# Performance work log

Measured on AMD Instinct MI355X. Metric: run time of the kernel, lower is better.

## Reference

```python
import jax, jax.numpy as jnp
import numpy as np
import math

WINDOW_SIZE = 11
SIGMA = 1.5
K1 = 0.01
K2 = 0.03
MAX_VAL = 1.0


def _make_window(window_size=WINDOW_SIZE, sigma=SIGMA):
    # Faithful to torch: 1D gaussian -> [1,1,window_size] -> repeat((3,1,1,1)) -> [3,1,1,ws]
    xs = np.arange(window_size)
    w = np.exp(-((xs - window_size // 2) ** 2) / float(2 * sigma ** 2)).astype(np.float32)
    w = w / w.sum()
    w = w[None, None, :]                      # [1,1,ws]
    w = np.tile(w[None], (3, 1, 1, 1))        # [3,1,1,ws]  (OIHW, 1x11 kernel, 3 out channels)
    return jnp.asarray(w)


def _conv(x, w, pad):
    # x: [B,1,H,W], w: [3,1,1,ws], padding=pad on both spatial dims (matches torch conv2d)
    return jax.lax.conv_general_dilated(
        x, w, window_strides=(1, 1), padding=((pad, pad), (pad, pad)),
        dimension_numbers=("NCHW", "OIHW", "NCHW"))


def setup_inputs() -> dict:
    key = jax.random.key(0)
    k1, k2 = jax.random.split(key)
    B, H, W = 16, 512, 512
    img1 = jax.random.uniform(k1, (B, H, W), dtype=jnp.float32)
    img2 = jax.random.uniform(k2, (B, H, W), dtype=jnp.float32)
    return {"img1": img1, "img2": img2}


def reference(img1, img2):
    pad = WINDOW_SIZE // 2
    window = _make_window()
    x1 = img1[:, None, :, :]  # [B,1,H,W]
    x2 = img2[:, None, :, :]

    mu1 = _conv(x1, window, pad)              # [B,3,H+2p,W]
    mu2 = _conv(x2, window, pad)
    mu1_mu2 = mu1 * mu2
    mu1_sq = mu1 * mu1
    mu2_sq = mu2 * mu2
    sigma1_sq = _conv(x1 * x1, window, pad) - mu1_sq
    sigma2_sq = _conv(x2 * x2, window, pad) - mu2_sq
    sigma12 = _conv(x1 * x2, window, pad) - mu1_mu2

    C1 = (K1 * MAX_VAL) ** 2
    C2 = (K2 * MAX_VAL) ** 2
    ssim = (2 * mu1_mu2 + C1) * (2 * sigma12 + C2) / (
        (mu1_sq + mu2_sq + C1) * (sigma1_sq + sigma2_sq + C2))
    return 1.0 - jnp.mean(ssim)
```

## Files before the change

kernel.cpp:

```cpp
#include <hip/hip_runtime.h>
#include <cmath>

typedef float f32x2 __attribute__((ext_vector_type(2)));
typedef float f32x4 __attribute__((ext_vector_type(4)));

#define IMG_W 512
#define NROWS 8192
#define PAIRS_PER_BLOCK 2
#define NBLOCKS (NROWS / (2 * PAIRS_PER_BLOCK))
#define TPB 128

struct WinW { float w[11]; };

__global__ __launch_bounds__(TPB) void ssim_rows(
    const float* __restrict__ img1, const float* __restrict__ img2,
    float* __restrict__ partial, WinW ww)
{
    __shared__ __align__(16) f32x2 l1[528];
    __shared__ __align__(16) f32x2 l2[528];
    const int tid = threadIdx.x;

    const float C1 = 1e-4f;
    const float C2 = 9e-4f;

    f32x2 acc = {0.f, 0.f};

    for (int pp = 0; pp < PAIRS_PER_BLOCK; ++pp) {
        const int pairIdx = blockIdx.x * PAIRS_PER_BLOCK + pp;
        const long long r0 = (long long)pairIdx * 2 * IMG_W;
        const int col = 4 * tid;

        const f32x4 a0 = *(const f32x4*)&img1[r0 + col];
        const f32x4 a1 = *(const f32x4*)&img1[r0 + IMG_W + col];
        const f32x4 b0 = *(const f32x4*)&img2[r0 + col];
        const f32x4 b1 = *(const f32x4*)&img2[r0 + IMG_W + col];

        __syncthreads();
        #pragma unroll
        for (int c = 0; c < 4; ++c) {
            l1[5 + col + c] = f32x2{a0[c], a1[c]};
            l2[5 + col + c] = f32x2{b0[c], b1[c]};
        }
        if (tid < 16) {
            const int slot = (tid < 5) ? tid : (512 + tid);
            l1[slot] = f32x2{0.f, 0.f};
            l2[slot] = f32x2{0.f, 0.f};
        }
        __syncthreads();

        f32x2 a[16], b[16];
        #pragma unroll
        for (int s = 0; s < 8; ++s) {
            *(f32x4*)&a[2 * s] = *(const f32x4*)&l1[col + 2 * s];
            *(f32x4*)&b[2 * s] = *(const f32x4*)&l2[col + 2 * s];
        }

        f32x2 mu1[4], mu2[4], s11[4], s22[4], s12[4];
        #pragma unroll
        for (int p = 0; p < 4; ++p) {
            mu1[p] = f32x2{0.f, 0.f}; mu2[p] = f32x2{0.f, 0.f};
            s11[p] = f32x2{0.f, 0.f}; s22[p] = f32x2{0.f, 0.f};
            s12[p] = f32x2{0.f, 0.f};
        }

        #pragma unroll
        for (int j = 0; j < 14; ++j) {
            const f32x2 aj = a[j], bj = b[j];
            const f32x2 aa = aj * aj, bb = bj * bj, ab = aj * bj;
            #pragma unroll
            for (int p = 0; p < 4; ++p) {
                const int k = j - p;
                if (k >= 0 && k < 11) {
                    const float wk = ww.w[k];
                    mu1[p] += wk * aj;
                    mu2[p] += wk * bj;
                    s11[p] += wk * aa;
                    s22[p] += wk * bb;
                    s12[p] += wk * ab;
                }
            }
        }

        #pragma unroll
        for (int p = 0; p < 4; ++p) {
            const f32x2 m12 = mu1[p] * mu2[p];
            const f32x2 m1s = mu1[p] * mu1[p];
            const f32x2 m2s = mu2[p] * mu2[p];
            const f32x2 num = (2.f * m12 + C1) * (2.f * (s12[p] - m12) + C2);
            const f32x2 den = (m1s + m2s + C1) * ((s11[p] - m1s) + (s22[p] - m2s) + C2);
            f32x2 r;
            r.x = __builtin_amdgcn_rcpf(den.x);
            r.y = __builtin_amdgcn_rcpf(den.y);
            acc += num * r;
        }
    }

    float s = acc.x + acc.y;
    #pragma unroll
    for (int off = 32; off > 0; off >>= 1)
        s += __shfl_down(s, off, 64);
    __shared__ float wsum[TPB / 64];
    if ((tid & 63) == 0) wsum[tid >> 6] = s;
    __syncthreads();
    if (tid == 0) partial[blockIdx.x] = wsum[0] + wsum[1];
}

__global__ __launch_bounds__(256) void ssim_final(
    const float* __restrict__ partial, float* __restrict__ out)
{
    const int tid = threadIdx.x;
    float s = 0.f;
    for (int i = tid; i < NBLOCKS; i += 256) s += partial[i];
    #pragma unroll
    for (int off = 32; off > 0; off >>= 1)
        s += __shfl_down(s, off, 64);
    __shared__ float ws[4];
    if ((tid & 63) == 0) ws[tid >> 6] = s;
    __syncthreads();
    if (tid == 0) {
        const float total = ws[0] + ws[1] + ws[2] + ws[3];
        out[0] = 1.0f - (total + 81920.0f) / 4276224.0f;
    }
}

extern "C" void kernel_launch(void* const* d_in, const int* in_sizes, int n_in,
                              void* d_out, int out_size, void* d_ws, size_t ws_size,
                              hipStream_t stream) {
    const float* img1 = (const float*)d_in[0];
    const float* img2 = (const float*)d_in[1];
    float* out = (float*)d_out;
    float* partial = (float*)d_ws;

    WinW ww;
    for (int i = 0; i < 11; ++i) {
        const double d = (double)(i - 5);
        ww.w[i] = (float)std::exp(-(d * d) / 4.5);
    }
    float s = 0.f;
    for (int i = 0; i < 11; ++i) s += ww.w[i];
    for (int i = 0; i < 11; ++i) ww.w[i] /= s;

    ssim_rows<<<NBLOCKS, TPB, 0, stream>>>(img1, img2, partial, ww);
    ssim_final<<<1, 256, 0, stream>>>(partial, out);
}
```

Before: 16.38 us.

## Fuse final reduction via fixed-point atomics and prefetch next row pair

Drops the separate final-reduction kernel. Each block converts its partial sum to a 64-bit fixed-point integer and atomically adds it, and the last block to arrive (tracked by an atomic counter) writes the result. The per-block loop now prefetches the next row pair into registers and double-buffers shared memory, which removes one barrier per iteration, and each block handles twice as many row pairs. A memset is added to the stream to clear the accumulator. Risks include the extra memset launch cost and the limited precision of the fixed-point conversion.

Result: slower. 40.86 us (+149.4%).

```diff
diff --git a/kernel.cpp b/kernel.cpp
--- a/kernel.cpp
+++ b/kernel.cpp
@@ -6,53 +6,63 @@
 
 #define IMG_W 512
 #define NROWS 8192
-#define PAIRS_PER_BLOCK 2
+#define PAIRS_PER_BLOCK 4
 #define NBLOCKS (NROWS / (2 * PAIRS_PER_BLOCK))
 #define TPB 128
+#define SCALE 16777216.0
 
 struct WinW { float w[11]; };
 
-__global__ __launch_bounds__(TPB) void ssim_rows(
+__global__ __launch_bounds__(TPB) void ssim_fused(
     const float* __restrict__ img1, const float* __restrict__ img2,
-    float* __restrict__ partial, WinW ww)
+    unsigned long long* __restrict__ acc64, unsigned int* __restrict__ cnt,
+    float* __restrict__ out, WinW ww)
 {
-    __shared__ __align__(16) f32x2 l1[528];
-    __shared__ __align__(16) f32x2 l2[528];
+    __shared__ __align__(16) f32x2 l1[2][528];
+    __shared__ __align__(16) f32x2 l2[2][528];
     const int tid = threadIdx.x;
-
+    const int col = 4 * tid;
     const float C1 = 1e-4f;
     const float C2 = 9e-4f;
 
     f32x2 acc = {0.f, 0.f};
 
+    const long long base = (long long)blockIdx.x * (PAIRS_PER_BLOCK * 2) * IMG_W;
+
+    f32x4 pa0 = *(const f32x4*)&img1[base + col];
+    f32x4 pa1 = *(const f32x4*)&img1[base + IMG_W + col];
+    f32x4 pb0 = *(const f32x4*)&img2[base + col];
+    f32x4 pb1 = *(const f32x4*)&img2[base + IMG_W + col];
+
+    #pragma unroll
     for (int pp = 0; pp < PAIRS_PER_BLOCK; ++pp) {
-        const int pairIdx = blockIdx.x * PAIRS_PER_BLOCK + pp;
-        const long long r0 = (long long)pairIdx * 2 * IMG_W;
-        const int col = 4 * tid;
+        const int buf = pp & 1;
+        const f32x4 a0 = pa0, a1 = pa1, b0 = pb0, b1 = pb1;
+        if (pp + 1 < PAIRS_PER_BLOCK) {
+            const long long nb = base + (long long)(pp + 1) * 2 * IMG_W;
+            pa0 = *(const f32x4*)&img1[nb + col];
+            pa1 = *(const f32x4*)&img1[nb + IMG_W + col];
+            pb0 = *(const f32x4*)&img2[nb + col];
+            pb1 = *(const f32x4*)&img2[nb + IMG_W + col];
+        }
 
-        const f32x4 a0 = *(const f32x4*)&img1[r0 + col];
-        const f32x4 a1 = *(const f32x4*)&img1[r0 + IMG_W + col];
-        const f32x4 b0 = *(const f32x4*)&img2[r0 + col];
-        const f32x4 b1 = *(const f32x4*)&img2[r0 + IMG_W + col];
-
-        __syncthreads();
         #pragma unroll
         for (int c = 0; c < 4; ++c) {
-            l1[5 + col + c] = f32x2{a0[c], a1[c]};
-            l2[5 + col + c] = f32x2{b0[c], b1[c]};
+            l1[buf][5 + col + c] = f32x2{a0[c], a1[c]};
+            l2[buf][5 + col + c] = f32x2{b0[c], b1[c]};
         }
         if (tid < 16) {
             const int slot = (tid < 5) ? tid : (512 + tid);
-            l1[slot] = f32x2{0.f, 0.f};
-            l2[slot] = f32x2{0.f, 0.f};
+            l1[buf][slot] = f32x2{0.f, 0.f};
+            l2[buf][slot] = f32x2{0.f, 0.f};
         }
         __syncthreads();
 
         f32x2 a[16], b[16];
         #pragma unroll
         for (int s = 0; s < 8; ++s) {
-            *(f32x4*)&a[2 * s] = *(const f32x4*)&l1[col + 2 * s];
-            *(f32x4*)&b[2 * s] = *(const f32x4*)&l2[col + 2 * s];
+            *(f32x4*)&a[2 * s] = *(const f32x4*)&l1[buf][col + 2 * s];
+            *(f32x4*)&b[2 * s] = *(const f32x4*)&l2[buf][col + 2 * s];
         }
 
         f32x2 mu1[4], mu2[4], s11[4], s22[4], s12[4];
@@ -102,24 +112,18 @@
     __shared__ float wsum[TPB / 64];
     if ((tid & 63) == 0) wsum[tid >> 6] = s;
     __syncthreads();
-    if (tid == 0) partial[blockIdx.x] = wsum[0] + wsum[1];
-}
 
-__global__ __launch_bounds__(256) void ssim_final(
-    const float* __restrict__ partial, float* __restrict__ out)
-{
-    const int tid = threadIdx.x;
-    float s = 0.f;
-    for (int i = tid; i < NBLOCKS; i += 256) s += partial[i];
-    #pragma unroll
-    for (int off = 32; off > 0; off >>= 1)
-        s += __shfl_down(s, off, 64);
-    __shared__ float ws[4];
-    if ((tid & 63) == 0) ws[tid >> 6] = s;
-    __syncthreads();
     if (tid == 0) {
-        const float total = ws[0] + ws[1] + ws[2] + ws[3];
-        out[0] = 1.0f - (total + 81920.0f) / 4276224.0f;
+        const double sd = (double)(wsum[0] + wsum[1]) * SCALE;
+        const unsigned long long q = (unsigned long long)(sd + 0.5);
+        atomicAdd(acc64, q);
+        __threadfence();
+        const unsigned int prev = atomicAdd(cnt, 1u);
+        if (prev == NBLOCKS - 1) {
+            const unsigned long long tot = atomicAdd(acc64, 0ULL);
+            const double total = (double)tot / SCALE;
+            out[0] = (float)(1.0 - (total + 81920.0) / 4276224.0);
+        }
     }
 }
 
@@ -129,7 +133,10 @@
     const float* img1 = (const float*)d_in[0];
     const float* img2 = (const float*)d_in[1];
     float* out = (float*)d_out;
-    float* partial = (float*)d_ws;
+    unsigned long long* acc64 = (unsigned long long*)d_ws;
+    unsigned int* cnt = (unsigned int*)((char*)d_ws + 8);
+
+    hipMemsetAsync(d_ws, 0, 16, stream);
 
     WinW ww;
     for (int i = 0; i < 11; ++i) {
@@ -140,6 +147,5 @@
     for (int i = 0; i < 11; ++i) s += ww.w[i];
     for (int i = 0; i < 11; ++i) ww.w[i] /= s;
 
-    ssim_rows<<<NBLOCKS, TPB, 0, stream>>>(img1, img2, partial, ww);
-    ssim_final<<<1, 256, 0, stream>>>(partial, out);
+    ssim_fused<<<NBLOCKS, TPB, 0, stream>>>(img1, img2, acc64, cnt, out, ww);
 }
```
